# Optimization experiments

Hardware: AMD Instinct MI355X
Metric: run time of the kernel (lower is better)

The kernel has to match this reference:

```python
import jax, jax.numpy as jnp
import numpy as np

KEY_DIM = 1024
VALUE_DIM = 1024
NUM_HEADS = 16
ORIGIN_SHAPE = (8, 16, 16)  # T, H, W video-token grid
LOCAL_BLOCKS = 3
B = 1
S = int(np.prod(ORIGIN_SHAPE))  # 2048
DH = KEY_DIM // NUM_HEADS       # 64
DV = VALUE_DIM // NUM_HEADS


def make_layout():
    """Vectorized equivalent of SparseAttention.make_layout (causal=True)."""
    shape = np.array(ORIGIN_SHAPE, dtype=np.int64)
    cum = np.concatenate([np.flip(np.cumprod(np.flip(shape)))[1:], [1]]).astype(np.int64)
    idx = np.arange(S, dtype=np.int64)
    coords = (idx[None, :] // cum[:, None]) % shape[:, None]  # [ndim, S]
    diff = idx[:, None] - idx[None, :]
    layout = (diff >= 0) & (diff <= LOCAL_BLOCKS)  # causal local window
    for d in range(len(ORIGIN_SHAPE) - 1):  # causal axial strides along dims 0..ndim-2
        same = np.ones((S, S), dtype=bool)
        for e in range(len(ORIGIN_SHAPE)):
            if e != d:
                same &= coords[e][:, None] == coords[e][None, :]
        layout |= same & (coords[d][None, :] <= coords[d][:, None])
    return layout  # [S, S] bool


def setup_inputs() -> dict:
    key = jax.random.key(0)
    ks = jax.random.split(key, 11)
    sc = 0.02
    inp = {
        "query": jax.random.normal(ks[0], (B, S, KEY_DIM), jnp.float32),
        "key":   jax.random.normal(ks[1], (B, S, KEY_DIM), jnp.float32),
        "value": jax.random.normal(ks[2], (B, S, VALUE_DIM), jnp.float32),
        "wq": sc * jax.random.normal(ks[3], (KEY_DIM, KEY_DIM), jnp.float32),
        "bq": jnp.zeros((KEY_DIM,), jnp.float32),
        "wk": sc * jax.random.normal(ks[4], (KEY_DIM, KEY_DIM), jnp.float32),
        "bk": jnp.zeros((KEY_DIM,), jnp.float32),
        "wv": sc * jax.random.normal(ks[5], (VALUE_DIM, VALUE_DIM), jnp.float32),
        "bv": jnp.zeros((VALUE_DIM,), jnp.float32),
        "wo": sc * jax.random.normal(ks[6], (VALUE_DIM, KEY_DIM), jnp.float32),
        "bo": jnp.zeros((KEY_DIM,), jnp.float32),
        "layout": jnp.asarray(make_layout(), jnp.int32)[None, None],  # [1,1,S,S]
    }
    return inp


def reference(query, key, value, wq, bq, wk, bk, wv, bv, wo, bo, layout):
    def split(x, d):  # [B,S,H*d] -> [B,H,S,d]
        return x.reshape(B, S, NUM_HEADS, d).transpose(0, 2, 1, 3)
    q = split(query @ wq + bq, DH)
    k = split(key @ wk + bk, DH)
    v = split(value @ wv + bv, DV)
    logits = jnp.einsum('bhsd,bhtd->bhst', q, k) / jnp.sqrt(jnp.float32(DH))
    logits = jnp.where(layout > 0, logits, jnp.float32(-1e9))
    attn = jax.nn.softmax(logits, axis=-1)  # matches tf.sparse.softmax over layout support
    out = jnp.einsum('bhst,bhtd->bhsd', attn, v)
    out = out.transpose(0, 2, 1, 3).reshape(B, S, VALUE_DIM)
    return out @ wo + bo
```

## Files before the change

kernel.cpp:

```cpp
#include <hip/hip_runtime.h>
#include <hip/hip_bf16.h>
#include <cstdint>
#include <math.h>

#define SEQ    2048
#define DMODEL 1024
#define NHEAD  16
#define DHEAD  64
#define NZPAD  32

typedef __bf16 bf16;
typedef __bf16 bf16x8 __attribute__((ext_vector_type(8)));
typedef float  f32x4  __attribute__((ext_vector_type(4)));

typedef __attribute__((address_space(3))) uint32_t lds_u32;
typedef __attribute__((address_space(1))) const uint32_t global_u32;

__device__ __forceinline__ void async_load16(const void* g, void* l) {
    __builtin_amdgcn_global_load_lds((global_u32*)g, (lds_u32*)l, 16, 0, 0);
}

__device__ __forceinline__ int support_idx(int s, int c, int tt, int hh,
                                           int cnt) {
    const int jA = c * 256 + (s & 255);
    const int jB = (s & 0x700) + (c - tt) * 16 + (s & 15);
    const int jC = s - (cnt - 1 - c);
    return c < tt ? jA : (c < tt + hh ? jB : (c < cnt ? jC : s));
}

#define CAST_BLOCKS 3072
#define TR_BLOCKS   4096

__global__ __launch_bounds__(256) void prep_kernel(
    const float* __restrict__ q, const float* __restrict__ k, const float* __restrict__ v,
    bf16* __restrict__ qx, bf16* __restrict__ kx, bf16* __restrict__ vx,
    const float* __restrict__ w0, const float* __restrict__ w1,
    const float* __restrict__ w2, const float* __restrict__ w3,
    bf16* __restrict__ t0, bf16* __restrict__ t1,
    bf16* __restrict__ t2, bf16* __restrict__ t3) {
    __shared__ float tile[32][33];
    const int bid = blockIdx.x;
    if (bid < CAST_BLOCKS) {
        const int z = bid >> 10;
        const float* src = (z == 0) ? q : (z == 1) ? k : v;
        bf16* dst        = (z == 0) ? qx : (z == 1) ? kx : vx;
        const int i = (bid & 1023) * 256 + threadIdx.x;
        const float4* s4 = (const float4*)src;
        float4 a = s4[i * 2 + 0];
        float4 b = s4[i * 2 + 1];
        bf16x8 o;
        o[0] = (bf16)a.x; o[1] = (bf16)a.y; o[2] = (bf16)a.z; o[3] = (bf16)a.w;
        o[4] = (bf16)b.x; o[5] = (bf16)b.y; o[6] = (bf16)b.z; o[7] = (bf16)b.w;
        ((bf16x8*)dst)[i] = o;
    } else {
        const int b = bid - CAST_BLOCKS;
        const int z = b >> 10, rem = b & 1023;
        const float* w = (z == 0) ? w0 : (z == 1) ? w1 : (z == 2) ? w2 : w3;
        bf16* t        = (z == 0) ? t0 : (z == 1) ? t1 : (z == 2) ? t2 : t3;
        const int tx = threadIdx.x & 31, ty = threadIdx.x >> 5;
        const int kbase = (rem >> 5) * 32, nbase = (rem & 31) * 32;
#pragma unroll
        for (int i = 0; i < 4; ++i)
            tile[ty + 8 * i][tx] = w[(size_t)(kbase + ty + 8 * i) * DMODEL + nbase + tx];
        __syncthreads();
#pragma unroll
        for (int i = 0; i < 4; ++i)
            t[(size_t)(nbase + ty + 8 * i) * DMODEL + kbase + tx] = (bf16)tile[tx][ty + 8 * i];
    }
}

__global__ __launch_bounds__(256) void proj3_kernel(
    const bf16* __restrict__ qx, const bf16* __restrict__ kx, const bf16* __restrict__ vx,
    const bf16* __restrict__ wqT, const bf16* __restrict__ wkT, const bf16* __restrict__ wvT,
    const float* __restrict__ bq, const float* __restrict__ bk, const float* __restrict__ bv,
    bf16* __restrict__ qp, bf16* __restrict__ kp, bf16* __restrict__ vp) {
    constexpr int K = 1024, N = 1024, BK = 64, TM = 64, MI = 2;
    constexpr int ACH = TM * (BK / 8);
    constexpr int TCH = ACH + 128 * (BK / 8);

    const int orig = blockIdx.x;
    const int flat = (orig & 7) * 96 + (orig >> 3);
    const int z = flat >> 8;
    const int rem = flat & 255;
    const int m0 = (rem >> 3) * TM, n0 = (rem & 7) * 128;

    const bf16* A   = (z == 0) ? qx : (z == 1) ? kx : vx;
    const bf16* BT  = (z == 0) ? wqT : (z == 1) ? wkT : wvT;
    const float* bi = (z == 0) ? bq : (z == 1) ? bk : bv;
    bf16* C         = (z == 0) ? qp : (z == 1) ? kp : vp;

    __shared__ bf16 sA[2][TM * BK];
    __shared__ bf16 sB[2][128 * BK];
    const int tid = threadIdx.x;
    const int w = tid >> 6, lane = tid & 63;
    const int wm = w >> 1, wn = w & 1;
    const int lr = lane & 15, quad = lane >> 4;

    f32x4 acc[MI][4] = {};
    float bia[4];
#pragma unroll
    for (int ni = 0; ni < 4; ++ni) bia[ni] = bi[n0 + wn * 64 + ni * 16 + lr];

    auto stage = [&](int buf, int kt) {
#pragma unroll
        for (int kk = 0; kk < TCH / 256; ++kk) {
            const int cb = kk * 256 + w * 64;
            const int p  = cb + lane;
            if (cb < ACH) {
                const int row = p >> 3, chl = p & 7;
                const int chg = chl ^ (row & 7);
                async_load16(A + (size_t)(m0 + row) * K + kt + chg * 8,
                             (char*)&sA[buf][0] + cb * 16);
            } else {
                const int p2 = p - ACH, row = p2 >> 3, chl = p2 & 7;
                const int chg = chl ^ (row & 7);
                async_load16(BT + (size_t)(n0 + row) * K + kt + chg * 8,
                             (char*)&sB[buf][0] + (cb - ACH) * 16);
            }
        }
    };

    stage(0, 0);
    stage(1, BK);
    int cur = 0;
    for (int kt = 0; kt < K; kt += BK) {
        if (kt + BK < K) {
            asm volatile("s_waitcnt vmcnt(6)" ::: "memory");
        } else {
            asm volatile("s_waitcnt vmcnt(0)" ::: "memory");
        }
        __builtin_amdgcn_s_barrier();
        __builtin_amdgcn_sched_barrier(0);
#pragma unroll
        for (int ks = 0; ks < 2; ++ks) {
            bf16x8 af[MI], bfr[4];
#pragma unroll
            for (int mi = 0; mi < MI; ++mi) {
                const int row = wm * (TM / 2) + mi * 16 + lr;
                af[mi] = *(const bf16x8*)
                    &sA[cur][row * BK + ((ks * 4 + quad) ^ (row & 7)) * 8];
            }
#pragma unroll
            for (int ni = 0; ni < 4; ++ni) {
                const int row = wn * 64 + ni * 16 + lr;
                bfr[ni] = *(const bf16x8*)
                    &sB[cur][row * BK + ((ks * 4 + quad) ^ (row & 7)) * 8];
            }
            __builtin_amdgcn_s_setprio(1);
#pragma unroll
            for (int mi = 0; mi < MI; ++mi)
#pragma unroll
                for (int ni = 0; ni < 4; ++ni)
                    acc[mi][ni] = __builtin_amdgcn_mfma_f32_16x16x32_bf16(
                        af[mi], bfr[ni], acc[mi][ni], 0, 0, 0);
            __builtin_amdgcn_s_setprio(0);
        }
        __builtin_amdgcn_s_barrier();
        __builtin_amdgcn_sched_barrier(0);
        if (kt + 2 * BK < K) stage(cur, kt + 2 * BK);
        cur ^= 1;
    }

#pragma unroll
    for (int mi = 0; mi < MI; ++mi)
#pragma unroll
        for (int ni = 0; ni < 4; ++ni) {
            const int row = m0 + wm * (TM / 2) + mi * 16 + quad * 4;
            const int col = n0 + wn * 64 + ni * 16 + lr;
            const f32x4 vv = acc[mi][ni];
#pragma unroll
            for (int r = 0; r < 4; ++r)
                C[(size_t)(row + r) * N + col] = (bf16)(vv[r] + bia[ni]);
        }
}

__global__ __launch_bounds__(256) void gemm_final_kernel(
    const bf16* __restrict__ A, const bf16* __restrict__ BT,
    const float* __restrict__ bias, float* __restrict__ C) {
    constexpr int K = 1024, N = 1024, BK = 64, TM = 32, MI = 2;
    constexpr int ACH = TM * (BK / 8);
    constexpr int TCH = ACH + 128 * (BK / 8);

    const int orig = blockIdx.x;
    const int flat = (orig & 7) * 64 + (orig >> 3);
    const int m0 = (flat >> 3) * TM, n0 = (flat & 7) * 128;

    __shared__ bf16 sA[2][TM * BK];
    __shared__ bf16 sB[2][128 * BK];
    const int tid = threadIdx.x;
    const int w = tid >> 6, lane = tid & 63;
    const int lr = lane & 15, quad = lane >> 4;

    f32x4 acc[MI][2] = {};
    float bia[2];
#pragma unroll
    for (int ni = 0; ni < 2; ++ni) bia[ni] = bias[n0 + w * 32 + ni * 16 + lr];

    auto stage = [&](int buf, int kt) {
#pragma unroll
        for (int kk = 0; kk < TCH / 256; ++kk) {
            const int cb = kk * 256 + w * 64;
            const int p = cb + lane;
            if (cb < ACH) {
                const int row = p >> 3, chl = p & 7;
                const int chg = chl ^ (row & 7);
                async_load16(A + (size_t)(m0 + row) * K + kt + chg * 8,
                             (char*)&sA[buf][0] + cb * 16);
            } else {
                const int p2 = p - ACH, row = p2 >> 3, chl = p2 & 7;
                const int chg = chl ^ (row & 7);
                async_load16(BT + (size_t)(n0 + row) * K + kt + chg * 8,
                             (char*)&sB[buf][0] + (cb - ACH) * 16);
            }
        }
    };

    stage(0, 0);
    stage(1, BK);
    int cur = 0;
    for (int kt = 0; kt < K; kt += BK) {
        if (kt + BK < K) {
            asm volatile("s_waitcnt vmcnt(5)" ::: "memory");
        } else {
            asm volatile("s_waitcnt vmcnt(0)" ::: "memory");
        }
        __builtin_amdgcn_s_barrier();
        __builtin_amdgcn_sched_barrier(0);
#pragma unroll
        for (int ks = 0; ks < 2; ++ks) {
            bf16x8 af[MI], bfr[2];
#pragma unroll
            for (int mi = 0; mi < MI; ++mi) {
                const int row = mi * 16 + lr;
                af[mi] = *(const bf16x8*)
                    &sA[cur][row * BK + ((ks * 4 + quad) ^ (row & 7)) * 8];
            }
#pragma unroll
            for (int ni = 0; ni < 2; ++ni) {
                const int row = w * 32 + ni * 16 + lr;
                bfr[ni] = *(const bf16x8*)
                    &sB[cur][row * BK + ((ks * 4 + quad) ^ (row & 7)) * 8];
            }
            __builtin_amdgcn_s_setprio(1);
#pragma unroll
            for (int mi = 0; mi < MI; ++mi)
#pragma unroll
                for (int ni = 0; ni < 2; ++ni)
                    acc[mi][ni] = __builtin_amdgcn_mfma_f32_16x16x32_bf16(
                        af[mi], bfr[ni], acc[mi][ni], 0, 0, 0);
            __builtin_amdgcn_s_setprio(0);
        }
        __builtin_amdgcn_s_barrier();
        __builtin_amdgcn_sched_barrier(0);
        if (kt + 2 * BK < K) stage(cur, kt + 2 * BK);
        cur ^= 1;
    }

#pragma unroll
    for (int mi = 0; mi < MI; ++mi)
#pragma unroll
        for (int ni = 0; ni < 2; ++ni) {
            const int row = m0 + mi * 16 + quad * 4;
            const int col = n0 + w * 32 + ni * 16 + lr;
            const f32x4 vv = acc[mi][ni];
#pragma unroll
            for (int r = 0; r < 4; ++r)
                C[(size_t)(row + r) * N + col] = vv[r] + bia[ni];
        }
}

__global__ __launch_bounds__(256) void attn_kernel(
    const bf16* __restrict__ qp, const bf16* __restrict__ kp, const bf16* __restrict__ vp,
    bf16* __restrict__ ao) {
    const int wv = threadIdx.x >> 6, lane = threadIdx.x & 63;
    constexpr int NB = NHEAD * SEQ / 4;
    const int bid = (blockIdx.x & 7) * (NB >> 3) + (blockIdx.x >> 3);
    const int p = bid * 4 + wv;
    const int s = __builtin_amdgcn_readfirstlane(p & (SEQ - 1));
    const int h = __builtin_amdgcn_readfirstlane(p >> 11);
    const int hbase = h * DHEAD;
    const int hoff = hbase + lane;

    const int tt = (s >> 8) & 7, hh = (s >> 4) & 15;
    const int win = (s < 3) ? s : 3;
    const int cnt = tt + hh + win + 1;

    int t[NZPAD];
#pragma unroll
    for (int c = 0; c < NZPAD; ++c) t[c] = support_idx(s, c, tt, hh, cnt);

    const int c_lane = lane & 31;
    const int fo = (lane >> 5) << 5;
    const int myT = support_idx(s, c_lane, tt, hh, cnt);

    const bf16x8* qrow = (const bf16x8*)(qp + (size_t)s * DMODEL + hbase + fo);
    const bf16x8* krow = (const bf16x8*)(kp + (size_t)myT * DMODEL + hbase + fo);
    bf16x8 qc[4], kc[4];
#pragma unroll
    for (int j = 0; j < 4; ++j) { qc[j] = qrow[j]; kc[j] = krow[j]; }

    float vvv[NZPAD];
#pragma unroll
    for (int c = 0; c < NZPAD; ++c)
        vvv[c] = (float)vp[(size_t)t[c] * DMODEL + hoff];

    float dot = 0.f;
    __builtin_amdgcn_s_setprio(1);
#pragma unroll
    for (int j = 0; j < 4; ++j)
#pragma unroll
        for (int e = 0; e < 8; ++e)
            dot = fmaf((float)qc[j][e], (float)kc[j][e], dot);
    __builtin_amdgcn_s_setprio(0);
    dot += __shfl_xor(dot, 32);

    const float logit = (c_lane < cnt) ? dot * 0.125f : -1e30f;
    float m = logit;
    m = fmaxf(m, __shfl_xor(m, 1)); m = fmaxf(m, __shfl_xor(m, 2));
    m = fmaxf(m, __shfl_xor(m, 4)); m = fmaxf(m, __shfl_xor(m, 8));
    m = fmaxf(m, __shfl_xor(m, 16));
    const float e = __expf(logit - m);
    float ssum = e;
    ssum += __shfl_xor(ssum, 1); ssum += __shfl_xor(ssum, 2);
    ssum += __shfl_xor(ssum, 4); ssum += __shfl_xor(ssum, 8);
    ssum += __shfl_xor(ssum, 16);
    const float prob = e / ssum;

    float acc = 0.f;
    __builtin_amdgcn_s_setprio(1);
#pragma unroll
    for (int c = 0; c < NZPAD; ++c) {
        const float pc = __uint_as_float(
            __builtin_amdgcn_readlane(__float_as_uint(prob), c));
        acc = fmaf(pc, vvv[c], acc);
    }
    __builtin_amdgcn_s_setprio(0);
    ao[(size_t)s * DMODEL + hoff] = (bf16)acc;
}

extern "C" void kernel_launch(void* const* d_in, const int* in_sizes, int n_in,
                              void* d_out, int out_size, void* d_ws, size_t ws_size,
                              hipStream_t stream) {
    const float* query = (const float*)d_in[0];
    const float* key   = (const float*)d_in[1];
    const float* value = (const float*)d_in[2];
    const float* wq = (const float*)d_in[3];
    const float* bq = (const float*)d_in[4];
    const float* wk = (const float*)d_in[5];
    const float* bk = (const float*)d_in[6];
    const float* wv = (const float*)d_in[7];
    const float* bv = (const float*)d_in[8];
    const float* wo = (const float*)d_in[9];
    const float* bo = (const float*)d_in[10];
    float* out = (float*)d_out;

    char* ws = (char*)d_ws;
    auto alloc = [&](size_t bytes) {
        char* p = ws;
        ws += (bytes + 255) & ~(size_t)255;
        return p;
    };
    bf16* qx  = (bf16*)alloc((size_t)SEQ * DMODEL * 2);
    bf16* kx  = (bf16*)alloc((size_t)SEQ * DMODEL * 2);
    bf16* vx  = (bf16*)alloc((size_t)SEQ * DMODEL * 2);
    bf16* wqT = (bf16*)alloc((size_t)DMODEL * DMODEL * 2);
    bf16* wkT = (bf16*)alloc((size_t)DMODEL * DMODEL * 2);
    bf16* wvT = (bf16*)alloc((size_t)DMODEL * DMODEL * 2);
    bf16* woT = (bf16*)alloc((size_t)DMODEL * DMODEL * 2);
    bf16* qp  = (bf16*)alloc((size_t)SEQ * DMODEL * 2);
    bf16* kp  = (bf16*)alloc((size_t)SEQ * DMODEL * 2);
    bf16* vp  = (bf16*)alloc((size_t)SEQ * DMODEL * 2);
    bf16* ao  = (bf16*)alloc((size_t)SEQ * DMODEL * 2);

    prep_kernel<<<dim3(CAST_BLOCKS + TR_BLOCKS), 256, 0, stream>>>(
        query, key, value, qx, kx, vx,
        wq, wk, wv, wo, wqT, wkT, wvT, woT);
    proj3_kernel<<<dim3(768), 256, 0, stream>>>(
        qx, kx, vx, wqT, wkT, wvT, bq, bk, bv, qp, kp, vp);
    attn_kernel<<<dim3(NHEAD * SEQ / 4), 256, 0, stream>>>(qp, kp, vp, ao);
    gemm_final_kernel<<<dim3(512), 256, 0, stream>>>(ao, woT, bo, out);
}
```

Baseline: 159.4 us.

## Fuse all four stages into one persistent cooperative kernel with grid syncs

Merges prep, QKV projection, sparse attention and output projection into one persistent cooperative mega-kernel. Blocks loop over each stage's tiles and are separated by grid-wide syncs, with a fallback to the original four launches if the cooperative launch fails. The aim is to remove per-launch overhead and the idle gaps between kernels. In exchange, every stage shares one 48KB LDS footprint, which limits occupancy, and the grid size is capped at 256 CUs times blocks per CU, so the attention stage runs many tiles per block instead of spreading across many small blocks.

```diff
diff --git a/kernel.cpp b/kernel.cpp
--- a/kernel.cpp
+++ b/kernel.cpp
@@ -1,13 +1,23 @@
 #include <hip/hip_runtime.h>
 #include <hip/hip_bf16.h>
+#include <hip/hip_cooperative_groups.h>
 #include <cstdint>
 #include <math.h>
+
+namespace cg = cooperative_groups;
 
 #define SEQ    2048
 #define DMODEL 1024
 #define NHEAD  16
 #define DHEAD  64
 #define NZPAD  32
+
+#define CAST_BLOCKS 3072
+#define TR_BLOCKS   4096
+#define PREP_WORK   (CAST_BLOCKS + TR_BLOCKS)
+#define PROJ_TILES  768
+#define ATTN_TILES  (NHEAD * SEQ / 4)
+#define FINAL_TILES 512
 
 typedef __bf16 bf16;
 typedef __bf16 bf16x8 __attribute__((ext_vector_type(8)));
@@ -28,23 +38,20 @@
     return c < tt ? jA : (c < tt + hh ? jB : (c < cnt ? jC : s));
 }
 
-#define CAST_BLOCKS 3072
-#define TR_BLOCKS   4096
-
-__global__ __launch_bounds__(256) void prep_kernel(
-    const float* __restrict__ q, const float* __restrict__ k, const float* __restrict__ v,
+
+__device__ __forceinline__ void prep_work(
+    int wid, const float* __restrict__ q, const float* __restrict__ k,
+    const float* __restrict__ v,
     bf16* __restrict__ qx, bf16* __restrict__ kx, bf16* __restrict__ vx,
     const float* __restrict__ w0, const float* __restrict__ w1,
     const float* __restrict__ w2, const float* __restrict__ w3,
     bf16* __restrict__ t0, bf16* __restrict__ t1,
-    bf16* __restrict__ t2, bf16* __restrict__ t3) {
-    __shared__ float tile[32][33];
-    const int bid = blockIdx.x;
-    if (bid < CAST_BLOCKS) {
-        const int z = bid >> 10;
+    bf16* __restrict__ t2, bf16* __restrict__ t3, char* ldsraw) {
+    if (wid < CAST_BLOCKS) {
+        const int z = wid >> 10;
         const float* src = (z == 0) ? q : (z == 1) ? k : v;
         bf16* dst        = (z == 0) ? qx : (z == 1) ? kx : vx;
-        const int i = (bid & 1023) * 256 + threadIdx.x;
+        const int i = (wid & 1023) * 256 + threadIdx.x;
         const float4* s4 = (const float4*)src;
         float4 a = s4[i * 2 + 0];
         float4 b = s4[i * 2 + 1];
@@ -53,7 +60,8 @@
         o[4] = (bf16)b.x; o[5] = (bf16)b.y; o[6] = (bf16)b.z; o[7] = (bf16)b.w;
         ((bf16x8*)dst)[i] = o;
     } else {
-        const int b = bid - CAST_BLOCKS;
+        float (*tile)[33] = (float(*)[33])ldsraw;
+        const int b = wid - CAST_BLOCKS;
         const int z = b >> 10, rem = b & 1023;
         const float* w = (z == 0) ? w0 : (z == 1) ? w1 : (z == 2) ? w2 : w3;
         bf16* t        = (z == 0) ? t0 : (z == 1) ? t1 : (z == 2) ? t2 : t3;
@@ -66,35 +74,40 @@
 #pragma unroll
         for (int i = 0; i < 4; ++i)
             t[(size_t)(nbase + ty + 8 * i) * DMODEL + kbase + tx] = (bf16)tile[tx][ty + 8 * i];
-    }
-}
-
-__global__ __launch_bounds__(256) void proj3_kernel(
-    const bf16* __restrict__ qx, const bf16* __restrict__ kx, const bf16* __restrict__ vx,
-    const bf16* __restrict__ wqT, const bf16* __restrict__ wkT, const bf16* __restrict__ wvT,
-    const float* __restrict__ bq, const float* __restrict__ bk, const float* __restrict__ bv,
-    bf16* __restrict__ qp, bf16* __restrict__ kp, bf16* __restrict__ vp) {
+        __syncthreads();
+    }
+}
+
+__device__ __forceinline__ void proj3_tile(
+    int tidx, const bf16* __restrict__ qx, const bf16* __restrict__ kx,
+    const bf16* __restrict__ vx,
+    const bf16* __restrict__ wqT, const bf16* __restrict__ wkT,
+    const bf16* __restrict__ wvT,
+    const float* __restrict__ bq, const float* __restrict__ bk,
+    const float* __restrict__ bv,
+    bf16* __restrict__ qp, bf16* __restrict__ kp, bf16* __restrict__ vp,
+    char* lds) {
     constexpr int K = 1024, N = 1024, BK = 64, TM = 64, MI = 2;
     constexpr int ACH = TM * (BK / 8);
     constexpr int TCH = ACH + 128 * (BK / 8);
 
-    const int orig = blockIdx.x;
-    const int flat = (orig & 7) * 96 + (orig >> 3);
-    const int z = flat >> 8;
-    const int rem = flat & 255;
-    const int m0 = (rem >> 3) * TM, n0 = (rem & 7) * 128;
+    const int n0 = (tidx & 7) * 128;
+    const int q_ = tidx >> 3;
+    const int z  = q_ >> 5;
+    const int m0 = (q_ & 31) * TM;
 
     const bf16* A   = (z == 0) ? qx : (z == 1) ? kx : vx;
     const bf16* BT  = (z == 0) ? wqT : (z == 1) ? wkT : wvT;
     const float* bi = (z == 0) ? bq : (z == 1) ? bk : bv;
     bf16* C         = (z == 0) ? qp : (z == 1) ? kp : vp;
 
-    __shared__ bf16 sA[2][TM * BK];
-    __shared__ bf16 sB[2][128 * BK];
     const int tid = threadIdx.x;
     const int w = tid >> 6, lane = tid & 63;
     const int wm = w >> 1, wn = w & 1;
     const int lr = lane & 15, quad = lane >> 4;
+
+    auto sAb = [&](int buf) { return lds + buf * (TM * BK * 2); };
+    auto sBb = [&](int buf) { return lds + 16384 + buf * (128 * BK * 2); };
 
     f32x4 acc[MI][4] = {};
     float bia[4];
@@ -110,12 +123,12 @@
                 const int row = p >> 3, chl = p & 7;
                 const int chg = chl ^ (row & 7);
                 async_load16(A + (size_t)(m0 + row) * K + kt + chg * 8,
-                             (char*)&sA[buf][0] + cb * 16);
+                             sAb(buf) + cb * 16);
             } else {
                 const int p2 = p - ACH, row = p2 >> 3, chl = p2 & 7;
                 const int chg = chl ^ (row & 7);
                 async_load16(BT + (size_t)(n0 + row) * K + kt + chg * 8,
-                             (char*)&sB[buf][0] + (cb - ACH) * 16);
+                             sBb(buf) + (cb - ACH) * 16);
             }
         }
     };
@@ -138,13 +151,13 @@
             for (int mi = 0; mi < MI; ++mi) {
                 const int row = wm * (TM / 2) + mi * 16 + lr;
                 af[mi] = *(const bf16x8*)
-                    &sA[cur][row * BK + ((ks * 4 + quad) ^ (row & 7)) * 8];
+                    (sAb(cur) + row * (BK * 2) + (((ks * 4 + quad) ^ (row & 7)) * 16));
             }
 #pragma unroll
             for (int ni = 0; ni < 4; ++ni) {
                 const int row = wn * 64 + ni * 16 + lr;
                 bfr[ni] = *(const bf16x8*)
-                    &sB[cur][row * BK + ((ks * 4 + quad) ^ (row & 7)) * 8];
+                    (sBb(cur) + row * (BK * 2) + (((ks * 4 + quad) ^ (row & 7)) * 16));
             }
             __builtin_amdgcn_s_setprio(1);
 #pragma unroll
@@ -174,107 +187,11 @@
         }
 }
 
-__global__ __launch_bounds__(256) void gemm_final_kernel(
-    const bf16* __restrict__ A, const bf16* __restrict__ BT,
-    const float* __restrict__ bias, float* __restrict__ C) {
-    constexpr int K = 1024, N = 1024, BK = 64, TM = 32, MI = 2;
-    constexpr int ACH = TM * (BK / 8);
-    constexpr int TCH = ACH + 128 * (BK / 8);
-
-    const int orig = blockIdx.x;
-    const int flat = (orig & 7) * 64 + (orig >> 3);
-    const int m0 = (flat >> 3) * TM, n0 = (flat & 7) * 128;
-
-    __shared__ bf16 sA[2][TM * BK];
-    __shared__ bf16 sB[2][128 * BK];
-    const int tid = threadIdx.x;
-    const int w = tid >> 6, lane = tid & 63;
-    const int lr = lane & 15, quad = lane >> 4;
-
-    f32x4 acc[MI][2] = {};
-    float bia[2];
-#pragma unroll
-    for (int ni = 0; ni < 2; ++ni) bia[ni] = bias[n0 + w * 32 + ni * 16 + lr];
-
-    auto stage = [&](int buf, int kt) {
-#pragma unroll
-        for (int kk = 0; kk < TCH / 256; ++kk) {
-            const int cb = kk * 256 + w * 64;
-            const int p = cb + lane;
-            if (cb < ACH) {
-                const int row = p >> 3, chl = p & 7;
-                const int chg = chl ^ (row & 7);
-                async_load16(A + (size_t)(m0 + row) * K + kt + chg * 8,
-                             (char*)&sA[buf][0] + cb * 16);
-            } else {
-                const int p2 = p - ACH, row = p2 >> 3, chl = p2 & 7;
-                const int chg = chl ^ (row & 7);
-                async_load16(BT + (size_t)(n0 + row) * K + kt + chg * 8,
-                             (char*)&sB[buf][0] + (cb - ACH) * 16);
-            }
-        }
-    };
-
-    stage(0, 0);
-    stage(1, BK);
-    int cur = 0;
-    for (int kt = 0; kt < K; kt += BK) {
-        if (kt + BK < K) {
-            asm volatile("s_waitcnt vmcnt(5)" ::: "memory");
-        } else {
-            asm volatile("s_waitcnt vmcnt(0)" ::: "memory");
-        }
-        __builtin_amdgcn_s_barrier();
-        __builtin_amdgcn_sched_barrier(0);
-#pragma unroll
-        for (int ks = 0; ks < 2; ++ks) {
-            bf16x8 af[MI], bfr[2];
-#pragma unroll
-            for (int mi = 0; mi < MI; ++mi) {
-                const int row = mi * 16 + lr;
-                af[mi] = *(const bf16x8*)
-                    &sA[cur][row * BK + ((ks * 4 + quad) ^ (row & 7)) * 8];
-            }
-#pragma unroll
-            for (int ni = 0; ni < 2; ++ni) {
-                const int row = w * 32 + ni * 16 + lr;
-                bfr[ni] = *(const bf16x8*)
-                    &sB[cur][row * BK + ((ks * 4 + quad) ^ (row & 7)) * 8];
-            }
-            __builtin_amdgcn_s_setprio(1);
-#pragma unroll
-            for (int mi = 0; mi < MI; ++mi)
-#pragma unroll
-                for (int ni = 0; ni < 2; ++ni)
-                    acc[mi][ni] = __builtin_amdgcn_mfma_f32_16x16x32_bf16(
-                        af[mi], bfr[ni], acc[mi][ni], 0, 0, 0);
-            __builtin_amdgcn_s_setprio(0);
-        }
-        __builtin_amdgcn_s_barrier();
-        __builtin_amdgcn_sched_barrier(0);
-        if (kt + 2 * BK < K) stage(cur, kt + 2 * BK);
-        cur ^= 1;
-    }
-
-#pragma unroll
-    for (int mi = 0; mi < MI; ++mi)
-#pragma unroll
-        for (int ni = 0; ni < 2; ++ni) {
-            const int row = m0 + mi * 16 + quad * 4;
-            const int col = n0 + w * 32 + ni * 16 + lr;
-            const f32x4 vv = acc[mi][ni];
-#pragma unroll
-            for (int r = 0; r < 4; ++r)
-                C[(size_t)(row + r) * N + col] = vv[r] + bia[ni];
-        }
-}
-
-__global__ __launch_bounds__(256) void attn_kernel(
-    const bf16* __restrict__ qp, const bf16* __restrict__ kp, const bf16* __restrict__ vp,
-    bf16* __restrict__ ao) {
+__device__ __forceinline__ void attn_tile(
+    int vb, const bf16* __restrict__ qp, const bf16* __restrict__ kp,
+    const bf16* __restrict__ vp, bf16* __restrict__ ao) {
     const int wv = threadIdx.x >> 6, lane = threadIdx.x & 63;
-    constexpr int NB = NHEAD * SEQ / 4;
-    const int bid = (blockIdx.x & 7) * (NB >> 3) + (blockIdx.x >> 3);
+    const int bid = (vb & 7) * (ATTN_TILES >> 3) + (vb >> 3);
     const int p = bid * 4 + wv;
     const int s = __builtin_amdgcn_readfirstlane(p & (SEQ - 1));
     const int h = __builtin_amdgcn_readfirstlane(p >> 11);
@@ -336,6 +253,157 @@
     }
     __builtin_amdgcn_s_setprio(0);
     ao[(size_t)s * DMODEL + hoff] = (bf16)acc;
+}
+
+__device__ __forceinline__ void final_tile(
+    int orig, const bf16* __restrict__ A, const bf16* __restrict__ BT,
+    const float* __restrict__ bias, float* __restrict__ C, char* lds) {
+    constexpr int K = 1024, N = 1024, BK = 64, TM = 32, MI = 2;
+    constexpr int ACH = TM * (BK / 8);
+    constexpr int TCH = ACH + 128 * (BK / 8);
+
+    const int flat = (orig & 7) * 64 + (orig >> 3);
+    const int m0 = (flat >> 3) * TM, n0 = (flat & 7) * 128;
+
+    const int tid = threadIdx.x;
+    const int w = tid >> 6, lane = tid & 63;
+    const int lr = lane & 15, quad = lane >> 4;
+
+    auto sAb = [&](int buf) { return lds + buf * (TM * BK * 2); };
+    auto sBb = [&](int buf) { return lds + 16384 + buf * (128 * BK * 2); };
+
+    f32x4 acc[MI][2] = {};
+    float bia[2];
+#pragma unroll
+    for (int ni = 0; ni < 2; ++ni) bia[ni] = bias[n0 + w * 32 + ni * 16 + lr];
+
+    auto stage = [&](int buf, int kt) {
+#pragma unroll
+        for (int kk = 0; kk < TCH / 256; ++kk) {
+            const int cb = kk * 256 + w * 64;
+            const int p = cb + lane;
+            if (cb < ACH) {
+                const int row = p >> 3, chl = p & 7;
+                const int chg = chl ^ (row & 7);
+                async_load16(A + (size_t)(m0 + row) * K + kt + chg * 8,
+                             sAb(buf) + cb * 16);
+            } else {
+                const int p2 = p - ACH, row = p2 >> 3, chl = p2 & 7;
+                const int chg = chl ^ (row & 7);
+                async_load16(BT + (size_t)(n0 + row) * K + kt + chg * 8,
+                             sBb(buf) + (cb - ACH) * 16);
+            }
+        }
+    };
+
+    stage(0, 0);
+    stage(1, BK);
+    int cur = 0;
+    for (int kt = 0; kt < K; kt += BK) {
+        if (kt + BK < K) {
+            asm volatile("s_waitcnt vmcnt(5)" ::: "memory");
+        } else {
+            asm volatile("s_waitcnt vmcnt(0)" ::: "memory");
+        }
+        __builtin_amdgcn_s_barrier();
+        __builtin_amdgcn_sched_barrier(0);
+#pragma unroll
+        for (int ks = 0; ks < 2; ++ks) {
+            bf16x8 af[MI], bfr[2];
+#pragma unroll
+            for (int mi = 0; mi < MI; ++mi) {
+                const int row = mi * 16 + lr;
+                af[mi] = *(const bf16x8*)
+                    (sAb(cur) + row * (BK * 2) + (((ks * 4 + quad) ^ (row & 7)) * 16));
+            }
+#pragma unroll
+            for (int ni = 0; ni < 2; ++ni) {
+                const int row = w * 32 + ni * 16 + lr;
+                bfr[ni] = *(const bf16x8*)
+                    (sBb(cur) + row * (BK * 2) + (((ks * 4 + quad) ^ (row & 7)) * 16));
+            }
+            __builtin_amdgcn_s_setprio(1);
+#pragma unroll
+            for (int mi = 0; mi < MI; ++mi)
+#pragma unroll
+                for (int ni = 0; ni < 2; ++ni)
+                    acc[mi][ni] = __builtin_amdgcn_mfma_f32_16x16x32_bf16(
+                        af[mi], bfr[ni], acc[mi][ni], 0, 0, 0);
+            __builtin_amdgcn_s_setprio(0);
+        }
+        __builtin_amdgcn_s_barrier();
+        __builtin_amdgcn_sched_barrier(0);
+        if (kt + 2 * BK < K) stage(cur, kt + 2 * BK);
+        cur ^= 1;
+    }
+
+#pragma unroll
+    for (int mi = 0; mi < MI; ++mi)
+#pragma unroll
+        for (int ni = 0; ni < 2; ++ni) {
+            const int row = m0 + mi * 16 + quad * 4;
+            const int col = n0 + w * 32 + ni * 16 + lr;
+            const f32x4 vv = acc[mi][ni];
+#pragma unroll
+            for (int r = 0; r < 4; ++r)
+                C[(size_t)(row + r) * N + col] = vv[r] + bia[ni];
+        }
+}
+
+__global__ __launch_bounds__(256) void mega_kernel(
+    const float* query, const float* key, const float* value,
+    const float* wq, const float* wk, const float* wv, const float* wo,
+    const float* bq, const float* bk, const float* bv, const float* bo,
+    bf16* qx, bf16* kx, bf16* vx,
+    bf16* wqT, bf16* wkT, bf16* wvT, bf16* woT,
+    bf16* qp, bf16* kp, bf16* vp, bf16* ao, float* out) {
+    __shared__ __align__(16) char lds[49152];
+    cg::grid_group grid = cg::this_grid();
+    const int G = gridDim.x;
+
+    for (int wid = blockIdx.x; wid < PREP_WORK; wid += G)
+        prep_work(wid, query, key, value, qx, kx, vx,
+                  wq, wk, wv, wo, wqT, wkT, wvT, woT, lds);
+    grid.sync();
+    for (int t = blockIdx.x; t < PROJ_TILES; t += G)
+        proj3_tile(t, qx, kx, vx, wqT, wkT, wvT, bq, bk, bv, qp, kp, vp, lds);
+    grid.sync();
+    for (int vb = blockIdx.x; vb < ATTN_TILES; vb += G)
+        attn_tile(vb, qp, kp, vp, ao);
+    grid.sync();
+    for (int t = blockIdx.x; t < FINAL_TILES; t += G)
+        final_tile(t, ao, woT, bo, out, lds);
+}
+
+__global__ __launch_bounds__(256) void prep_kernel(
+    const float* query, const float* key, const float* value,
+    bf16* qx, bf16* kx, bf16* vx,
+    const float* wq, const float* wk, const float* wv, const float* wo,
+    bf16* wqT, bf16* wkT, bf16* wvT, bf16* woT) {
+    __shared__ __align__(16) char lds[4352];
+    prep_work(blockIdx.x, query, key, value, qx, kx, vx,
+              wq, wk, wv, wo, wqT, wkT, wvT, woT, lds);
+}
+
+__global__ __launch_bounds__(256) void proj3_kernel(
+    const bf16* qx, const bf16* kx, const bf16* vx,
+    const bf16* wqT, const bf16* wkT, const bf16* wvT,
+    const float* bq, const float* bk, const float* bv,
+    bf16* qp, bf16* kp, bf16* vp) {
+    __shared__ __align__(16) char lds[49152];
+    proj3_tile(blockIdx.x, qx, kx, vx, wqT, wkT, wvT, bq, bk, bv,
+               qp, kp, vp, lds);
+}
+
+__global__ __launch_bounds__(256) void attn_kernel(
+    const bf16* qp, const bf16* kp, const bf16* vp, bf16* ao) {
+    attn_tile(blockIdx.x, qp, kp, vp, ao);
+}
+
+__global__ __launch_bounds__(256) void gemm_final_kernel(
+    const bf16* A, const bf16* BT, const float* bias, float* C) {
+    __shared__ __align__(16) char lds[49152];
+    final_tile(blockIdx.x, A, BT, bias, C, lds);
 }
 
 extern "C" void kernel_launch(void* const* d_in, const int* in_sizes, int n_in,
@@ -372,11 +440,40 @@
     bf16* vp  = (bf16*)alloc((size_t)SEQ * DMODEL * 2);
     bf16* ao  = (bf16*)alloc((size_t)SEQ * DMODEL * 2);
 
-    prep_kernel<<<dim3(CAST_BLOCKS + TR_BLOCKS), 256, 0, stream>>>(
-        query, key, value, qx, kx, vx,
-        wq, wk, wv, wo, wqT, wkT, wvT, woT);
-    proj3_kernel<<<dim3(768), 256, 0, stream>>>(
+    static int gridblks = 0;
+    static int coop = -1;
+    if (gridblks == 0) {
+        int mb = 0;
+        if (hipOccupancyMaxActiveBlocksPerMultiprocessor(&mb, mega_kernel, 256, 0)
+                != hipSuccess || mb < 1)
+            mb = 1;
+        long g = (long)mb * 256;
+        if (g > PROJ_TILES) g = PROJ_TILES;
+        gridblks = (int)g;
+    }
+
+    if (coop != 0) {
+        const float *a0 = query, *a1 = key, *a2 = value;
+        const float *a3 = wq, *a4 = wk, *a5 = wv, *a6 = wo;
+        const float *a7 = bq, *a8 = bk, *a9 = bv, *a10 = bo;
+        bf16 *a11 = qx, *a12 = kx, *a13 = vx;
+        bf16 *a14 = wqT, *a15 = wkT, *a16 = wvT, *a17 = woT;
+        bf16 *a18 = qp, *a19 = kp, *a20 = vp, *a21 = ao;
+        float* a22 = out;
+        void* args[] = {&a0, &a1, &a2, &a3, &a4, &a5, &a6, &a7, &a8, &a9, &a10,
+                        &a11, &a12, &a13, &a14, &a15, &a16, &a17,
+                        &a18, &a19, &a20, &a21, &a22};
+        hipError_t e = hipLaunchCooperativeKernel(
+            (const void*)mega_kernel, dim3(gridblks), dim3(256), args, 0, stream);
+        if (e == hipSuccess) { coop = 1; return; }
+        coop = 0;
+        (void)hipGetLastError();
+    }
+
+    prep_kernel<<<dim3(PREP_WORK), 256, 0, stream>>>(
+        query, key, value, qx, kx, vx, wq, wk, wv, wo, wqT, wkT, wvT, woT);
+    proj3_kernel<<<dim3(PROJ_TILES), 256, 0, stream>>>(
         qx, kx, vx, wqT, wkT, wvT, bq, bk, bv, qp, kp, vp);
-    attn_kernel<<<dim3(NHEAD * SEQ / 4), 256, 0, stream>>>(qp, kp, vp, ao);
-    gemm_final_kernel<<<dim3(512), 256, 0, stream>>>(ao, woT, bo, out);
-}
+    attn_kernel<<<dim3(ATTN_TILES), 256, 0, stream>>>(qp, kp, vp, ao);
+    gemm_final_kernel<<<dim3(FINAL_TILES), 256, 0, stream>>>(ao, woT, bo, out);
+}
```

Measured after the change: 327.8 us. +105.6%, slower.
